# Performance work log

Measured on AMD Instinct MI355X. Metric: run time of the kernel, lower is better.

The kernel has to match this reference:

```python
import jax, jax.numpy as jnp
import numpy as np

DIM = 768
GP_NUM = 49


def setup_inputs() -> dict:
    key = jax.random.key(0)
    ks = jax.random.split(key, 7)
    b, n, d = 8, 2048, DIM
    s = d ** -0.5
    x = jax.random.normal(ks[0], (b, n, d), dtype=jnp.float32)
    W_qkv = jax.random.normal(ks[1], (d, 3 * d), dtype=jnp.float32) * s
    b_qkv = jnp.zeros((3 * d,), dtype=jnp.float32)
    W_proj = jax.random.normal(ks[2], (d, d), dtype=jnp.float32) * s
    b_proj = jnp.zeros((d,), dtype=jnp.float32)
    W_gp = jax.random.normal(ks[3], (d, GP_NUM), dtype=jnp.float32) * s
    alpha = jax.random.normal(ks[4], (), dtype=jnp.float32)
    return {"x": x, "W_qkv": W_qkv, "b_qkv": b_qkv, "W_proj": W_proj,
            "b_proj": b_proj, "W_gp": W_gp, "alpha": alpha}


def reference(x, W_qkv, b_qkv, W_proj, b_proj, W_gp, alpha):
    d = x.shape[-1]
    scale = d ** -0.5
    qkv = x @ W_qkv + b_qkv            # [b, n, 3d]
    q, k, v = jnp.split(qkv, 3, axis=-1)
    # full n x n attention scores
    attn_scores = jnp.einsum('bnd,bmd->bnm', q, k) * scale
    # group affinity: softmax(gelu(v @ W_gp)) then outer product over groups
    gw = jax.nn.softmax(jax.nn.gelu(v @ W_gp, approximate=False), axis=-1)  # [b, n, g]
    group_weight = jnp.einsum('bng,bmg->bnm', gw, gw)  # [b, n, n]
    attn_scores = jax.nn.softmax(attn_scores * group_weight, axis=-1)
    a = jax.nn.sigmoid(alpha)
    attn_weights = (1.0 - a) * attn_scores + a * group_weight
    out = jnp.einsum('bnm,bmd->bnd', attn_weights, v)
    return out @ W_proj + b_proj
```

## Files before the change

### kernel.cpp

```cpp
#include <hip/hip_runtime.h>
#include <hip/hip_bf16.h>
#include <math.h>

#define CB 8
#define CN 2048
#define CD 768
#define CDQKV 2304
#define NG 49

typedef unsigned short ushort_t;
typedef __attribute__((ext_vector_type(8))) short bf16x8;
typedef __attribute__((ext_vector_type(4))) float f32x4;

__device__ __forceinline__ float bf2f(ushort_t u) {
    unsigned int x = ((unsigned int)u) << 16;
    return __builtin_bit_cast(float, x);
}
__device__ __forceinline__ ushort_t f2bf(float f) {
    unsigned int u = __builtin_bit_cast(unsigned int, f);
    u += 0x7fff + ((u >> 16) & 1);
    return (ushort_t)(u >> 16);
}
__device__ __forceinline__ ushort_t f2h(float f) {
    _Float16 h = (_Float16)f;
    return __builtin_bit_cast(ushort_t, h);
}
__device__ __forceinline__ float h2f(ushort_t u) {
    return (float)__builtin_bit_cast(_Float16, u);
}
__device__ __forceinline__ float sigmoidf_(float x) { return 1.f / (1.f + __expf(-x)); }

__device__ __forceinline__ void gload_lds16(const ushort_t* g, ushort_t* l) {
    __builtin_amdgcn_global_load_lds((const __attribute__((address_space(1))) void*)g,
                                     (__attribute__((address_space(3))) void*)l, 16, 0, 0);
}

__global__ void ws_fail_marker(float* out) {
    if (threadIdx.x == 0 && blockIdx.x == 0) out[0] = 31337.0f;
}

__global__ __launch_bounds__(256) void cast_bf16(const float* __restrict__ X,
                                                 ushort_t* __restrict__ XB, int n)
{
    int i = (blockIdx.x * 256 + threadIdx.x) * 8;
    if (i >= n) return;
    float4 a = *(const float4*)(X + i);
    float4 b = *(const float4*)(X + i + 4);
    ushort_t t[8];
    t[0] = f2bf(a.x); t[1] = f2bf(a.y); t[2] = f2bf(a.z); t[3] = f2bf(a.w);
    t[4] = f2bf(b.x); t[5] = f2bf(b.y); t[6] = f2bf(b.z); t[7] = f2bf(b.w);
    *(uint4*)(XB + i) = *(uint4*)t;
}

__global__ __launch_bounds__(256) void wt_kernel(const float* __restrict__ W,
                                                 ushort_t* __restrict__ WT,
                                                 int rows, int cols)
{
    __shared__ ushort_t tile[64][72];
    const int bx = blockIdx.x, by = blockIdx.y;
    const int t = threadIdx.x;
    const int r = t >> 2, cp = (t & 3) * 16;
    const float* src = W + (size_t)(by * 64 + r) * cols + bx * 64 + cp;
    ushort_t tmp[16];
#pragma unroll
    for (int i = 0; i < 16; i += 4) {
        float4 v = *(const float4*)(src + i);
        tmp[i + 0] = f2bf(v.x); tmp[i + 1] = f2bf(v.y);
        tmp[i + 2] = f2bf(v.z); tmp[i + 3] = f2bf(v.w);
    }
    *(uint4*)&tile[r][cp] = *(uint4*)tmp;
    *(uint4*)&tile[r][cp + 8] = *(uint4*)(tmp + 8);
    __syncthreads();
#pragma unroll
    for (int i = 0; i < 16; i++) tmp[i] = tile[cp + i][r];
    ushort_t* dst = WT + (size_t)(bx * 64 + r) * rows + by * 64 + cp;
    *(uint4*)dst = *(uint4*)tmp;
    *(uint4*)(dst + 8) = *(uint4*)(tmp + 8);
}

__global__ __launch_bounds__(256) void wgpt_kernel(const float* __restrict__ Wg,
                                                   ushort_t* __restrict__ WGPT)
{
    int idx = blockIdx.x * 256 + threadIdx.x;
    if (idx >= 64 * CD) return;
    int gg = idx / CD, k = idx % CD;
    WGPT[idx] = (gg < NG) ? f2bf(Wg[(size_t)k * NG + gg]) : (ushort_t)0;
}

#define GEN_STAGE(dstA_, dstB_, kt_, Abase_, Bbase_, lda_, ldb_) do {          \
    _Pragma("unroll")                                                          \
    for (int _p = 0; _p < 4; _p++) {                                           \
        int _idx = _p * 256 + tid;                                             \
        int _row = _idx >> 3;                                                  \
        int _lsl = (_idx & 7) ^ (_row & 7);                                    \
        gload_lds16((Abase_) + (size_t)_row * (lda_) + (size_t)(kt_) * 64 + _lsl * 8, \
                    (dstA_) + _idx * 8);                                       \
        gload_lds16((Bbase_) + (size_t)_row * (ldb_) + (size_t)(kt_) * 64 + _lsl * 8, \
                    (dstB_) + _idx * 8);                                       \
    } } while (0)

#define G_COMPUTE(srcA_, srcB_) do {                                           \
    _Pragma("unroll")                                                          \
    for (int _ks = 0; _ks < 2; _ks++) {                                        \
        bf16x8 _af[4], _bf[4];                                                 \
        _Pragma("unroll")                                                      \
        for (int _f = 0; _f < 4; _f++) {                                       \
            int _ra = wr * 64 + _f * 16 + c;                                   \
            int _pa = (_ks * 4 + g) ^ (_ra & 7);                               \
            _af[_f] = *(const bf16x8*)((srcA_) + _ra * 64 + _pa * 8);          \
            int _rb = wc * 64 + _f * 16 + c;                                   \
            int _pb = (_ks * 4 + g) ^ (_rb & 7);                               \
            _bf[_f] = *(const bf16x8*)((srcB_) + _rb * 64 + _pb * 8);          \
        }                                                                      \
        _Pragma("unroll")                                                      \
        for (int _mf = 0; _mf < 4; _mf++)                                      \
            _Pragma("unroll")                                                  \
            for (int _nf = 0; _nf < 4; _nf++)                                  \
                acc[_mf * 4 + _nf] = __builtin_amdgcn_mfma_f32_16x16x32_bf16(  \
                    _af[_mf], _bf[_nf], acc[_mf * 4 + _nf], 0, 0, 0);          \
    } } while (0)

#define STAGE_A128(dst_, base_, ld_, kt_) do {                                 \
    _Pragma("unroll")                                                          \
    for (int _p = 0; _p < 4; _p++) {                                           \
        int _idx = _p * 256 + tid;                                             \
        int _row = _idx >> 3;                                                  \
        int _lsl = (_idx & 7) ^ (_row & 7);                                    \
        gload_lds16((base_) + (size_t)_row * (ld_) + (size_t)(kt_) * 64 + _lsl * 8, \
                    (dst_) + _idx * 8);                                        \
    } } while (0)

#define STAGE_B64(dst_, base_, ld_, kt_) do {                                  \
    _Pragma("unroll")                                                          \
    for (int _p = 0; _p < 2; _p++) {                                           \
        int _idx = _p * 256 + tid;                                             \
        int _row = _idx >> 3;                                                  \
        int _lsl = (_idx & 7) ^ (_row & 7);                                    \
        gload_lds16((base_) + (size_t)_row * (ld_) + (size_t)(kt_) * 64 + _lsl * 8, \
                    (dst_) + _idx * 8);                                        \
    } } while (0)

#define N64_COMPUTE(srcA_, srcB_) do {                                         \
    _Pragma("unroll")                                                          \
    for (int _ks = 0; _ks < 2; _ks++) {                                        \
        bf16x8 _af[2], _bf[4];                                                 \
        _Pragma("unroll")                                                      \
        for (int _f = 0; _f < 2; _f++) {                                       \
            int _ra = w * 32 + _f * 16 + c;                                    \
            int _pa = (_ks * 4 + g) ^ (_ra & 7);                               \
            _af[_f] = *(const bf16x8*)((srcA_) + _ra * 64 + _pa * 8);          \
        }                                                                      \
        _Pragma("unroll")                                                      \
        for (int _f = 0; _f < 4; _f++) {                                       \
            int _rb = _f * 16 + c;                                             \
            int _pb = (_ks * 4 + g) ^ (_rb & 7);                               \
            _bf[_f] = *(const bf16x8*)((srcB_) + _rb * 64 + _pb * 8);          \
        }                                                                      \
        _Pragma("unroll")                                                      \
        for (int _mf = 0; _mf < 2; _mf++)                                      \
            _Pragma("unroll")                                                  \
            for (int _nf = 0; _nf < 4; _nf++)                                  \
                acc[_mf * 4 + _nf] = __builtin_amdgcn_mfma_f32_16x16x32_bf16(  \
                    _af[_mf], _bf[_nf], acc[_mf * 4 + _nf], 0, 0, 0);          \
    } } while (0)

template <int OUTMODE>
__global__ __launch_bounds__(256, 2) void mfma_gemm(
    const ushort_t* __restrict__ Ag, const ushort_t* __restrict__ Bg,
    const float* __restrict__ bias,
    ushort_t* __restrict__ Qd, ushort_t* __restrict__ Kd, ushort_t* __restrict__ Vd,
    float* __restrict__ OUT)
{
    __shared__ __align__(16) ushort_t As[2][128 * 64];
    __shared__ __align__(16) ushort_t Bs[2][128 * 64];
    const int tid = threadIdx.x;
    const int lane = tid & 63;
    const int w = tid >> 6;
    const int c = lane & 15, g = lane >> 4;
    const int wr = w >> 1, wc = w & 1;
    const int m0 = blockIdx.x * 128;
    const int n0 = blockIdx.y * 128;
    const ushort_t* Ab = Ag + (size_t)m0 * CD;
    const ushort_t* Bb = Bg + (size_t)n0 * CD;

    f32x4 acc[16];
#pragma unroll
    for (int i = 0; i < 16; i++) acc[i] = (f32x4){0.f, 0.f, 0.f, 0.f};

    GEN_STAGE(As[0], Bs[0], 0, Ab, Bb, CD, CD);
    __syncthreads();
#pragma unroll 1
    for (int kt = 0; kt < 12; kt++) {
        const int cur = kt & 1;
        if (kt < 11) GEN_STAGE(As[cur ^ 1], Bs[cur ^ 1], kt + 1, Ab, Bb, CD, CD);
        G_COMPUTE(As[cur], Bs[cur]);
        __syncthreads();
    }

    if (OUTMODE == 0) {
        const int seg = n0 / CD;
        const int nl0 = n0 % CD;
        ushort_t* dst = (seg == 0) ? Qd : (seg == 1) ? Kd : Vd;
#pragma unroll
        for (int nf = 0; nf < 4; nf++) {
            float bv = bias[n0 + wc * 64 + nf * 16 + c];
            int n = nl0 + wc * 64 + nf * 16 + c;
#pragma unroll
            for (int mf = 0; mf < 4; mf++) {
#pragma unroll
                for (int r = 0; r < 4; r++) {
                    int m = m0 + wr * 64 + mf * 16 + g * 4 + r;
                    dst[(size_t)m * CD + n] = f2bf(acc[mf * 4 + nf][r] + bv);
                }
            }
        }
    } else {
#pragma unroll
        for (int nf = 0; nf < 4; nf++) {
            int n = n0 + wc * 64 + nf * 16 + c;
            float bv = bias[n];
#pragma unroll
            for (int mf = 0; mf < 4; mf++) {
#pragma unroll
                for (int r = 0; r < 4; r++) {
                    int m = m0 + wr * 64 + mf * 16 + g * 4 + r;
                    OUT[(size_t)m * CD + n] = acc[mf * 4 + nf][r] + bv;
                }
            }
        }
    }
}

__global__ __launch_bounds__(256, 2) void gw_gemm(
    const ushort_t* __restrict__ Vb, const ushort_t* __restrict__ WGPT,
    ushort_t* __restrict__ GWP, ushort_t* __restrict__ GWT)
{
    __shared__ __align__(16) ushort_t As[2][128 * 64];
    __shared__ __align__(16) ushort_t Bs[2][64 * 64];
    const int tid = threadIdx.x;
    const int lane = tid & 63;
    const int w = tid >> 6;
    const int c = lane & 15, g = lane >> 4;
    const int row0 = blockIdx.x * 128;
    const ushort_t* Ab = Vb + (size_t)row0 * CD;

    f32x4 acc[8];
#pragma unroll
    for (int i = 0; i < 8; i++) acc[i] = (f32x4){0.f, 0.f, 0.f, 0.f};

    STAGE_A128(As[0], Ab, CD, 0);
    STAGE_B64(Bs[0], WGPT, CD, 0);
    __syncthreads();
#pragma unroll 1
    for (int kt = 0; kt < 12; kt++) {
        const int cur = kt & 1;
        if (kt < 11) {
            STAGE_A128(As[cur ^ 1], Ab, CD, kt + 1);
            STAGE_B64(Bs[cur ^ 1], WGPT, CD, kt + 1);
        }
        N64_COMPUTE(As[cur], Bs[cur]);
        __syncthreads();
    }

    float gl[2][4][4];
#pragma unroll
    for (int mf = 0; mf < 2; mf++)
#pragma unroll
        for (int nf = 0; nf < 4; nf++) {
            int col = nf * 16 + c;
#pragma unroll
            for (int rr = 0; rr < 4; rr++) {
                float xx = acc[mf * 4 + nf][rr];
                float ge = 0.5f * xx * (1.f + erff(xx * 0.7071067811865475f));
                gl[mf][nf][rr] = (col < NG) ? ge : -1e30f;
            }
        }
#pragma unroll
    for (int mf = 0; mf < 2; mf++) {
#pragma unroll
        for (int rr = 0; rr < 4; rr++) {
            float m = fmaxf(fmaxf(gl[mf][0][rr], gl[mf][1][rr]),
                            fmaxf(gl[mf][2][rr], gl[mf][3][rr]));
#pragma unroll
            for (int s = 1; s < 16; s <<= 1) m = fmaxf(m, __shfl_xor(m, s, 64));
            float ssum = 0.f;
#pragma unroll
            for (int nf = 0; nf < 4; nf++) {
                int col = nf * 16 + c;
                float e = (col < NG) ? __expf(gl[mf][nf][rr] - m) : 0.f;
                gl[mf][nf][rr] = e;
                ssum += e;
            }
#pragma unroll
            for (int s = 1; s < 16; s <<= 1) ssum += __shfl_xor(ssum, s, 64);
            float inv = 1.f / ssum;
            int row = row0 + w * 32 + mf * 16 + g * 4 + rr;
            int bb = row >> 11, nn = row & 2047;
#pragma unroll
            for (int nf = 0; nf < 4; nf++) {
                int col = nf * 16 + c;
                ushort_t wv = f2bf(gl[mf][nf][rr] * inv);
                GWP[(size_t)row * 64 + col] = wv;
                GWT[((size_t)bb * 64 + col) * CN + nn] = wv;
            }
        }
    }
}

__global__ __launch_bounds__(256, 2) void z_gemm(
    const ushort_t* __restrict__ VT, const ushort_t* __restrict__ GWT,
    ushort_t* __restrict__ ZT)
{
    __shared__ __align__(16) ushort_t As[2][128 * 64];
    __shared__ __align__(16) ushort_t Bs[2][64 * 64];
    const int tid = threadIdx.x;
    const int lane = tid & 63;
    const int w = tid >> 6;
    const int c = lane & 15, g = lane >> 4;
    const int b = blockIdx.y;
    const int m0 = blockIdx.x * 128;
    const ushort_t* Ab = VT + ((size_t)b * CD + m0) * CN;
    const ushort_t* Bb = GWT + (size_t)b * 64 * CN;

    f32x4 acc[8];
#pragma unroll
    for (int i = 0; i < 8; i++) acc[i] = (f32x4){0.f, 0.f, 0.f, 0.f};

    STAGE_A128(As[0], Ab, CN, 0);
    STAGE_B64(Bs[0], Bb, CN, 0);
    __syncthreads();
#pragma unroll 1
    for (int kt = 0; kt < 32; kt++) {
        const int cur = kt & 1;
        if (kt < 31) {
            STAGE_A128(As[cur ^ 1], Ab, CN, kt + 1);
            STAGE_B64(Bs[cur ^ 1], Bb, CN, kt + 1);
        }
        N64_COMPUTE(As[cur], Bs[cur]);
        __syncthreads();
    }

#pragma unroll
    for (int mf = 0; mf < 2; mf++)
#pragma unroll
        for (int nf = 0; nf < 4; nf++) {
            int col = nf * 16 + c;
#pragma unroll
            for (int rr = 0; rr < 4; rr++) {
                int row = m0 + w * 32 + mf * 16 + g * 4 + rr;
                ZT[((size_t)b * CD + row) * 64 + col] = f2bf(acc[mf * 4 + nf][rr]);
            }
        }
}

__global__ __launch_bounds__(256, 2) void s_gemm(
    const ushort_t* __restrict__ Qb, const ushort_t* __restrict__ Kb,
    const ushort_t* __restrict__ GWP, ushort_t* __restrict__ S)
{
    __shared__ __align__(16) ushort_t As[2][128 * 64];
    __shared__ __align__(16) ushort_t Bs[2][128 * 64];
    const int tid = threadIdx.x;
    const int lane = tid & 63;
    const int w = tid >> 6;
    const int c = lane & 15, g = lane >> 4;
    const int wr = w >> 1, wc = w & 1;
    const int b = blockIdx.z;
    const int m0 = blockIdx.x * 128;
    const int n0 = blockIdx.y * 128;
    const ushort_t* Ab = Qb + ((size_t)b * CN + m0) * CD;
    const ushort_t* Bb = Kb + ((size_t)b * CN + n0) * CD;

    f32x4 acc[16], gacc[16];
#pragma unroll
    for (int i = 0; i < 16; i++) {
        acc[i] = (f32x4){0.f, 0.f, 0.f, 0.f};
        gacc[i] = (f32x4){0.f, 0.f, 0.f, 0.f};
    }

    GEN_STAGE(As[0], Bs[0], 0, Ab, Bb, CD, CD);

    {
        const ushort_t* Gq = GWP + ((size_t)b * CN + m0) * 64;
        const ushort_t* Gk = GWP + ((size_t)b * CN + n0) * 64;
        bf16x8 gqf[2][4], gkf[2][4];
#pragma unroll
        for (int ks = 0; ks < 2; ks++)
#pragma unroll
            for (int f = 0; f < 4; f++) {
                gqf[ks][f] = *(const bf16x8*)(Gq + (size_t)(wr * 64 + f * 16 + c) * 64 + ks * 32 + g * 8);
                gkf[ks][f] = *(const bf16x8*)(Gk + (size_t)(wc * 64 + f * 16 + c) * 64 + ks * 32 + g * 8);
            }
#pragma unroll
        for (int ks = 0; ks < 2; ks++)
#pragma unroll
            for (int mf = 0; mf < 4; mf++)
#pragma unroll
                for (int nf = 0; nf < 4; nf++)
                    gacc[mf * 4 + nf] = __builtin_amdgcn_mfma_f32_16x16x32_bf16(
                        gqf[ks][mf], gkf[ks][nf], gacc[mf * 4 + nf], 0, 0, 0);
    }

    __syncthreads();
#pragma unroll 1
    for (int kt = 0; kt < 12; kt++) {
        const int cur = kt & 1;
        if (kt < 11) GEN_STAGE(As[cur ^ 1], Bs[cur ^ 1], kt + 1, Ab, Bb, CD, CD);
        G_COMPUTE(As[cur], Bs[cur]);
        __syncthreads();
    }

    ushort_t* Sb = S + ((size_t)b * CN + m0) * CN + n0;
    const float scale = 0.03608439182435161f;
#pragma unroll
    for (int nf = 0; nf < 4; nf++) {
        int n = wc * 64 + nf * 16 + c;
#pragma unroll
        for (int mf = 0; mf < 4; mf++) {
#pragma unroll
            for (int r = 0; r < 4; r++) {
                int m = wr * 64 + mf * 16 + g * 4 + r;
                float z = acc[mf * 4 + nf][r] * scale * gacc[mf * 4 + nf][r];
                Sb[(size_t)m * CN + n] = f2h(z);
            }
        }
    }
}

__global__ __launch_bounds__(256) void softmax_rows(ushort_t* __restrict__ SP)
{
    const int lane = threadIdx.x & 63;
    const int row = blockIdx.x * 4 + (threadIdx.x >> 6);
    ushort_t* rp = SP + (size_t)row * CN;

    float v[32];
    float mx = -1e30f;
#pragma unroll
    for (int ch = 0; ch < 4; ch++) {
        uint4 u = *(const uint4*)(rp + ch * 512 + lane * 8);
        const unsigned int uu[4] = {u.x, u.y, u.z, u.w};
#pragma unroll
        for (int j = 0; j < 4; j++) {
            float a = h2f((ushort_t)(uu[j] & 0xffff));
            float bq = h2f((ushort_t)(uu[j] >> 16));
            v[ch * 8 + j * 2] = a;
            v[ch * 8 + j * 2 + 1] = bq;
            mx = fmaxf(mx, fmaxf(a, bq));
        }
    }
#pragma unroll
    for (int s = 32; s > 0; s >>= 1) mx = fmaxf(mx, __shfl_xor(mx, s, 64));
    float sum = 0.f;
#pragma unroll
    for (int i = 0; i < 32; i++) {
        v[i] = __expf(v[i] - mx);
        sum += v[i];
    }
#pragma unroll
    for (int s = 32; s > 0; s >>= 1) sum += __shfl_xor(sum, s, 64);
    float inv = 1.f / sum;
#pragma unroll
    for (int ch = 0; ch < 4; ch++) {
        ushort_t t[8];
#pragma unroll
        for (int j = 0; j < 8; j++) t[j] = f2bf(v[ch * 8 + j] * inv);
        *(uint4*)(rp + ch * 512 + lane * 8) = *(uint4*)t;
    }
}

__global__ __launch_bounds__(256, 2) void pv_gemm(
    const ushort_t* __restrict__ P, const ushort_t* __restrict__ VT,
    const ushort_t* __restrict__ GWP, const ushort_t* __restrict__ ZT,
    const float* __restrict__ alpha_p, ushort_t* __restrict__ OP)
{
    __shared__ __align__(16) ushort_t As[2][128 * 64];
    __shared__ __align__(16) ushort_t Bs[2][128 * 64];
    const int tid = threadIdx.x;
    const int lane = tid & 63;
    const int w = tid >> 6;
    const int c = lane & 15, g = lane >> 4;
    const int wr = w >> 1, wc = w & 1;
    const int b = blockIdx.z;
    const int m0 = blockIdx.x * 128;
    const int n0 = blockIdx.y * 128;
    const ushort_t* Ab = P + ((size_t)b * CN + m0) * CN;
    const ushort_t* Bb = VT + ((size_t)b * CD + n0) * CN;

    f32x4 acc[16], zacc[16];
#pragma unroll
    for (int i = 0; i < 16; i++) {
        acc[i] = (f32x4){0.f, 0.f, 0.f, 0.f};
        zacc[i] = (f32x4){0.f, 0.f, 0.f, 0.f};
    }

    GEN_STAGE(As[0], Bs[0], 0, Ab, Bb, CN, CN);

    {
        const ushort_t* Gq = GWP + ((size_t)b * CN + m0) * 64;
        const ushort_t* Zt = ZT + (size_t)b * CD * 64;
        bf16x8 zaf[2][4], zbf[2][4];
#pragma unroll
        for (int ks = 0; ks < 2; ks++)
#pragma unroll
            for (int f = 0; f < 4; f++) {
                zaf[ks][f] = *(const bf16x8*)(Gq + (size_t)(wr * 64 + f * 16 + c) * 64 + ks * 32 + g * 8);
                zbf[ks][f] = *(const bf16x8*)(Zt + (size_t)(n0 + wc * 64 + f * 16 + c) * 64 + ks * 32 + g * 8);
            }
#pragma unroll
        for (int ks = 0; ks < 2; ks++)
#pragma unroll
            for (int mf = 0; mf < 4; mf++)
#pragma unroll
                for (int nf = 0; nf < 4; nf++)
                    zacc[mf * 4 + nf] = __builtin_amdgcn_mfma_f32_16x16x32_bf16(
                        zaf[ks][mf], zbf[ks][nf], zacc[mf * 4 + nf], 0, 0, 0);
    }

    __syncthreads();
#pragma unroll 1
    for (int kt = 0; kt < 32; kt++) {
        const int cur = kt & 1;
        if (kt < 31) GEN_STAGE(As[cur ^ 1], Bs[cur ^ 1], kt + 1, Ab, Bb, CN, CN);
        G_COMPUTE(As[cur], Bs[cur]);
        __syncthreads();
    }

    const float aa = sigmoidf_(alpha_p[0]);
    ushort_t* OPb = OP + ((size_t)b * CN + m0) * CD;
#pragma unroll
    for (int nf = 0; nf < 4; nf++) {
        int n = n0 + wc * 64 + nf * 16 + c;
#pragma unroll
        for (int mf = 0; mf < 4; mf++) {
#pragma unroll
            for (int r = 0; r < 4; r++) {
                int m = wr * 64 + mf * 16 + g * 4 + r;
                OPb[(size_t)m * CD + n] =
                    f2bf((1.f - aa) * acc[mf * 4 + nf][r] + aa * zacc[mf * 4 + nf][r]);
            }
        }
    }
}

__global__ __launch_bounds__(256) void vt_transpose(const ushort_t* __restrict__ VB,
                                                    ushort_t* __restrict__ VT)
{
    __shared__ ushort_t tile[64][72];
    const int bx = blockIdx.x, by = blockIdx.y, b = blockIdx.z;
    const int t = threadIdx.x;
    const int r = t >> 2, cp = (t & 3) * 16;
    const ushort_t* src = VB + ((size_t)b * CN + bx * 64 + r) * CD + by * 64 + cp;
    *(uint4*)&tile[r][cp] = *(const uint4*)src;
    *(uint4*)&tile[r][cp + 8] = *(const uint4*)(src + 8);
    __syncthreads();
    ushort_t tmp[16];
#pragma unroll
    for (int i = 0; i < 16; i++) tmp[i] = tile[cp + i][r];
    ushort_t* dst = VT + ((size_t)b * CD + by * 64 + r) * CN + bx * 64 + cp;
    *(uint4*)dst = *(uint4*)tmp;
    *(uint4*)(dst + 8) = *(uint4*)(tmp + 8);
}

extern "C" void kernel_launch(void* const* d_in, const int* in_sizes, int n_in,
                              void* d_out, int out_size, void* d_ws, size_t ws_size,
                              hipStream_t stream) {
    const float* x      = (const float*)d_in[0];
    const float* W_qkv  = (const float*)d_in[1];
    const float* b_qkv  = (const float*)d_in[2];
    const float* W_proj = (const float*)d_in[3];
    const float* b_proj = (const float*)d_in[4];
    const float* W_gp   = (const float*)d_in[5];
    const float* alpha  = (const float*)d_in[6];
    float* out = (float*)d_out;

    const size_t BND    = (size_t)CB * CN * CD;
    const size_t SZ_BF  = BND * 2;
    const size_t SZ_WPT = (size_t)CD * CD * 2;
    const size_t SZ_GWP = (size_t)CB * CN * 64 * 2;
    const size_t SZ_GWT = (size_t)CB * 64 * CN * 2;
    const size_t SZ_ZT  = (size_t)CB * CD * 64 * 2;
    const size_t SZ_WGPT= (size_t)64 * CD * 2;
    const size_t SZ_SP  = (size_t)CB * CN * CN * 2;
    const size_t need = 5 * SZ_BF + SZ_WPT + SZ_GWP + SZ_GWT + SZ_ZT + SZ_WGPT + SZ_SP;
    if (ws_size < need) {
        ws_fail_marker<<<1, 1, 0, stream>>>(out);
        return;
    }
    char* p = (char*)d_ws;
    ushort_t* qb   = (ushort_t*)p; p += SZ_BF;
    ushort_t* kb   = (ushort_t*)p; p += SZ_BF;
    ushort_t* vb   = (ushort_t*)p; p += SZ_BF;
    ushort_t* vt   = (ushort_t*)p; p += SZ_BF;
    ushort_t* opb  = (ushort_t*)p; p += SZ_BF;
    ushort_t* wpt  = (ushort_t*)p; p += SZ_WPT;
    ushort_t* gwp  = (ushort_t*)p; p += SZ_GWP;
    ushort_t* gwt  = (ushort_t*)p; p += SZ_GWT;
    ushort_t* zt   = (ushort_t*)p; p += SZ_ZT;
    ushort_t* wgpt = (ushort_t*)p; p += SZ_WGPT;
    ushort_t* sp   = (ushort_t*)p; p += SZ_SP;
    ushort_t* xb  = sp;
    ushort_t* wqt = sp + BND;

    cast_bf16<<<dim3((int)(BND / 8 / 256)), 256, 0, stream>>>(x, xb, (int)BND);
    wt_kernel<<<dim3(36, 12), 256, 0, stream>>>(W_qkv, wqt, CD, CDQKV);
    wt_kernel<<<dim3(12, 12), 256, 0, stream>>>(W_proj, wpt, CD, CD);
    wgpt_kernel<<<dim3(192), 256, 0, stream>>>(W_gp, wgpt);
    mfma_gemm<0><<<dim3(128, 18), 256, 0, stream>>>(xb, wqt, b_qkv, qb, kb, vb, nullptr);
    gw_gemm<<<dim3(128), 256, 0, stream>>>(vb, wgpt, gwp, gwt);
    vt_transpose<<<dim3(32, 12, 8), 256, 0, stream>>>(vb, vt);
    z_gemm<<<dim3(6, 8), 256, 0, stream>>>(vt, gwt, zt);
    s_gemm<<<dim3(16, 16, 8), 256, 0, stream>>>(qb, kb, gwp, sp);
    softmax_rows<<<dim3(4096), 256, 0, stream>>>(sp);
    pv_gemm<<<dim3(16, 6, 8), 256, 0, stream>>>(sp, vt, gwp, zt, alpha, opb);
    mfma_gemm<1><<<dim3(128, 6), 256, 0, stream>>>(opb, wpt, b_proj, nullptr, nullptr, nullptr, out);
}
```

Baseline: 364.2 us.

## Fold group term into PV GEMM via padded K and use 256x256 GEMM tiles

Adds a 256x256-tile, 512-thread bf16 MFMA GEMM with a two-stage prefetch, explicit waitcnt barriers, priority hints and XCD-aware block remapping. It replaces the QKV, PV and output projection GEMMs. The softmax now scales by (1-a) and writes a*gw into 64 extra columns of a padded score buffer (row stride 2112). z_gemm writes into matching padded columns of V^T, so the group-weight contribution becomes part of a single K=2112 GEMM instead of a separate fused pass. The larger tiles should raise reuse, at the cost of fewer blocks (192 for PV and projection) and heavier register and LDS pressure.

Result: no change. 361.0 us (-0.9%).

```diff
diff --git a/kernel.cpp b/kernel.cpp
--- a/kernel.cpp
+++ b/kernel.cpp
@@ -7,6 +7,7 @@
 #define CD 768
 #define CDQKV 2304
 #define NG 49
+#define SLD 2112
 
 typedef unsigned short ushort_t;
 typedef __attribute__((ext_vector_type(8))) short bf16x8;
@@ -85,6 +86,143 @@
     if (idx >= 64 * CD) return;
     int gg = idx / CD, k = idx % CD;
     WGPT[idx] = (gg < NG) ? f2bf(Wg[(size_t)k * NG + gg]) : (ushort_t)0;
+}
+
+#define STAGE256(dstA_, dstB_, kt_) do {                                       \
+    _Pragma("unroll")                                                          \
+    for (int _p = 0; _p < 4; _p++) {                                           \
+        int _idx = _p * 512 + tid;                                             \
+        int _row = _idx >> 3;                                                  \
+        int _lsl = (_idx & 7) ^ (_row & 7);                                    \
+        gload_lds16(Ab + (size_t)_row * LDA + (size_t)(kt_) * 64 + _lsl * 8,   \
+                    (dstA_) + _idx * 8);                                       \
+    }                                                                          \
+    _Pragma("unroll")                                                          \
+    for (int _p = 0; _p < 4; _p++) {                                           \
+        int _idx = _p * 512 + tid;                                             \
+        int _row = _idx >> 3;                                                  \
+        int _lsl = (_idx & 7) ^ (_row & 7);                                    \
+        gload_lds16(Bb + (size_t)_row * LDB + (size_t)(kt_) * 64 + _lsl * 8,   \
+                    (dstB_) + _idx * 8);                                       \
+    } } while (0)
+
+template <int OUTMODE, int NK, int LDA, int LDB>
+__global__ __launch_bounds__(512, 2) void gemm256(
+    const ushort_t* __restrict__ Ag, const ushort_t* __restrict__ Bg,
+    const float* __restrict__ bias,
+    ushort_t* __restrict__ Qd, ushort_t* __restrict__ Kd, ushort_t* __restrict__ Vd,
+    ushort_t* __restrict__ OB, float* __restrict__ OF)
+{
+    __shared__ __align__(16) ushort_t bufA[2][256 * 64];
+    __shared__ __align__(16) ushort_t bufB[2][256 * 64];
+
+    const int tid = threadIdx.x;
+    const int lane = tid & 63;
+    const int w = tid >> 6;
+    const int c = lane & 15, g = lane >> 4;
+    const int wr = w >> 2, wc = w & 3;
+
+    const int per = gridDim.x >> 3;
+    const int idx = (blockIdx.x & 7) * per + (blockIdx.x >> 3);
+    const int mb = idx & 63;
+    const int nb = idx >> 6;
+    const int m0 = mb * 256;
+    const int n0 = nb * 256;
+
+    const ushort_t* Ab = Ag + (size_t)m0 * LDA;
+    const ushort_t* Bb = (OUTMODE == 2)
+        ? Bg + ((size_t)(m0 >> 11) * CD + n0) * LDB
+        : Bg + (size_t)n0 * LDB;
+
+    f32x4 acc[8][4];
+#pragma unroll
+    for (int i = 0; i < 8; i++)
+#pragma unroll
+        for (int j = 0; j < 4; j++) acc[i][j] = (f32x4){0.f, 0.f, 0.f, 0.f};
+
+    STAGE256(bufA[0], bufB[0], 0);
+    STAGE256(bufA[1], bufB[1], 1);
+
+#pragma unroll 1
+    for (int kt = 0; kt < NK; kt++) {
+        const int cur = kt & 1;
+        asm volatile("s_waitcnt vmcnt(8)" ::: "memory");
+        __builtin_amdgcn_s_barrier();
+
+        bf16x8 af[2][8], bf[2][4];
+#pragma unroll
+        for (int ks = 0; ks < 2; ks++) {
+#pragma unroll
+            for (int mf = 0; mf < 8; mf++) {
+                int ra = wr * 128 + mf * 16 + c;
+                int pa = (ks * 4 + g) ^ (ra & 7);
+                af[ks][mf] = *(const bf16x8*)(&bufA[cur][0] + ra * 64 + pa * 8);
+            }
+#pragma unroll
+            for (int nf = 0; nf < 4; nf++) {
+                int rb = wc * 64 + nf * 16 + c;
+                int pb = (ks * 4 + g) ^ (rb & 7);
+                bf[ks][nf] = *(const bf16x8*)(&bufB[cur][0] + rb * 64 + pb * 8);
+            }
+        }
+        asm volatile("s_waitcnt lgkmcnt(0)" ::: "memory");
+        __builtin_amdgcn_s_barrier();
+        if (kt + 2 < NK) STAGE256(bufA[cur], bufB[cur], kt + 2);
+
+        __builtin_amdgcn_s_setprio(1);
+#pragma unroll
+        for (int ks = 0; ks < 2; ks++)
+#pragma unroll
+            for (int mf = 0; mf < 8; mf++)
+#pragma unroll
+                for (int nf = 0; nf < 4; nf++)
+                    acc[mf][nf] = __builtin_amdgcn_mfma_f32_16x16x32_bf16(
+                        af[ks][mf], bf[ks][nf], acc[mf][nf], 0, 0, 0);
+        __builtin_amdgcn_s_setprio(0);
+    }
+
+    if (OUTMODE == 0) {
+        const int seg = n0 / CD;
+        const int nl0 = n0 % CD;
+        ushort_t* dst = (seg == 0) ? Qd : (seg == 1) ? Kd : Vd;
+#pragma unroll
+        for (int nf = 0; nf < 4; nf++) {
+            float bv = bias[n0 + wc * 64 + nf * 16 + c];
+            int n = nl0 + wc * 64 + nf * 16 + c;
+#pragma unroll
+            for (int mf = 0; mf < 8; mf++)
+#pragma unroll
+                for (int r = 0; r < 4; r++) {
+                    int m = m0 + wr * 128 + mf * 16 + g * 4 + r;
+                    dst[(size_t)m * CD + n] = f2bf(acc[mf][nf][r] + bv);
+                }
+        }
+    } else if (OUTMODE == 1) {
+#pragma unroll
+        for (int nf = 0; nf < 4; nf++) {
+            int n = n0 + wc * 64 + nf * 16 + c;
+            float bv = bias[n];
+#pragma unroll
+            for (int mf = 0; mf < 8; mf++)
+#pragma unroll
+                for (int r = 0; r < 4; r++) {
+                    int m = m0 + wr * 128 + mf * 16 + g * 4 + r;
+                    OF[(size_t)m * CD + n] = acc[mf][nf][r] + bv;
+                }
+        }
+    } else {
+#pragma unroll
+        for (int nf = 0; nf < 4; nf++) {
+            int n = n0 + wc * 64 + nf * 16 + c;
+#pragma unroll
+            for (int mf = 0; mf < 8; mf++)
+#pragma unroll
+                for (int r = 0; r < 4; r++) {
+                    int m = m0 + wr * 128 + mf * 16 + g * 4 + r;
+                    OB[(size_t)m * CD + n] = f2bf(acc[mf][nf][r]);
+                }
+        }
+    }
 }
 
 #define GEN_STAGE(dstA_, dstB_, kt_, Abase_, Bbase_, lda_, ldb_) do {          \
@@ -164,73 +302,6 @@
                     _af[_mf], _bf[_nf], acc[_mf * 4 + _nf], 0, 0, 0);          \
     } } while (0)
 
-template <int OUTMODE>
-__global__ __launch_bounds__(256, 2) void mfma_gemm(
-    const ushort_t* __restrict__ Ag, const ushort_t* __restrict__ Bg,
-    const float* __restrict__ bias,
-    ushort_t* __restrict__ Qd, ushort_t* __restrict__ Kd, ushort_t* __restrict__ Vd,
-    float* __restrict__ OUT)
-{
-    __shared__ __align__(16) ushort_t As[2][128 * 64];
-    __shared__ __align__(16) ushort_t Bs[2][128 * 64];
-    const int tid = threadIdx.x;
-    const int lane = tid & 63;
-    const int w = tid >> 6;
-    const int c = lane & 15, g = lane >> 4;
-    const int wr = w >> 1, wc = w & 1;
-    const int m0 = blockIdx.x * 128;
-    const int n0 = blockIdx.y * 128;
-    const ushort_t* Ab = Ag + (size_t)m0 * CD;
-    const ushort_t* Bb = Bg + (size_t)n0 * CD;
-
-    f32x4 acc[16];
-#pragma unroll
-    for (int i = 0; i < 16; i++) acc[i] = (f32x4){0.f, 0.f, 0.f, 0.f};
-
-    GEN_STAGE(As[0], Bs[0], 0, Ab, Bb, CD, CD);
-    __syncthreads();
-#pragma unroll 1
-    for (int kt = 0; kt < 12; kt++) {
-        const int cur = kt & 1;
-        if (kt < 11) GEN_STAGE(As[cur ^ 1], Bs[cur ^ 1], kt + 1, Ab, Bb, CD, CD);
-        G_COMPUTE(As[cur], Bs[cur]);
-        __syncthreads();
-    }
-
-    if (OUTMODE == 0) {
-        const int seg = n0 / CD;
-        const int nl0 = n0 % CD;
-        ushort_t* dst = (seg == 0) ? Qd : (seg == 1) ? Kd : Vd;
-#pragma unroll
-        for (int nf = 0; nf < 4; nf++) {
-            float bv = bias[n0 + wc * 64 + nf * 16 + c];
-            int n = nl0 + wc * 64 + nf * 16 + c;
-#pragma unroll
-            for (int mf = 0; mf < 4; mf++) {
-#pragma unroll
-                for (int r = 0; r < 4; r++) {
-                    int m = m0 + wr * 64 + mf * 16 + g * 4 + r;
-                    dst[(size_t)m * CD + n] = f2bf(acc[mf * 4 + nf][r] + bv);
-                }
-            }
-        }
-    } else {
-#pragma unroll
-        for (int nf = 0; nf < 4; nf++) {
-            int n = n0 + wc * 64 + nf * 16 + c;
-            float bv = bias[n];
-#pragma unroll
-            for (int mf = 0; mf < 4; mf++) {
-#pragma unroll
-                for (int r = 0; r < 4; r++) {
-                    int m = m0 + wr * 64 + mf * 16 + g * 4 + r;
-                    OUT[(size_t)m * CD + n] = acc[mf * 4 + nf][r] + bv;
-                }
-            }
-        }
-    }
-}
-
 __global__ __launch_bounds__(256, 2) void gw_gemm(
     const ushort_t* __restrict__ Vb, const ushort_t* __restrict__ WGPT,
     ushort_t* __restrict__ GWP, ushort_t* __restrict__ GWT)
@@ -308,8 +379,7 @@
 }
 
 __global__ __launch_bounds__(256, 2) void z_gemm(
-    const ushort_t* __restrict__ VT, const ushort_t* __restrict__ GWT,
-    ushort_t* __restrict__ ZT)
+    ushort_t* __restrict__ VTt, const ushort_t* __restrict__ GWT)
 {
     __shared__ __align__(16) ushort_t As[2][128 * 64];
     __shared__ __align__(16) ushort_t Bs[2][64 * 64];
@@ -319,21 +389,21 @@
     const int c = lane & 15, g = lane >> 4;
     const int b = blockIdx.y;
     const int m0 = blockIdx.x * 128;
-    const ushort_t* Ab = VT + ((size_t)b * CD + m0) * CN;
+    const ushort_t* Ab = VTt + ((size_t)b * CD + m0) * SLD;
     const ushort_t* Bb = GWT + (size_t)b * 64 * CN;
 
     f32x4 acc[8];
 #pragma unroll
     for (int i = 0; i < 8; i++) acc[i] = (f32x4){0.f, 0.f, 0.f, 0.f};
 
-    STAGE_A128(As[0], Ab, CN, 0);
+    STAGE_A128(As[0], Ab, SLD, 0);
     STAGE_B64(Bs[0], Bb, CN, 0);
     __syncthreads();
 #pragma unroll 1
     for (int kt = 0; kt < 32; kt++) {
         const int cur = kt & 1;
         if (kt < 31) {
-            STAGE_A128(As[cur ^ 1], Ab, CN, kt + 1);
+            STAGE_A128(As[cur ^ 1], Ab, SLD, kt + 1);
             STAGE_B64(Bs[cur ^ 1], Bb, CN, kt + 1);
         }
         N64_COMPUTE(As[cur], Bs[cur]);
@@ -348,7 +418,7 @@
 #pragma unroll
             for (int rr = 0; rr < 4; rr++) {
                 int row = m0 + w * 32 + mf * 16 + g * 4 + rr;
-                ZT[((size_t)b * CD + row) * 64 + col] = f2bf(acc[mf * 4 + nf][rr]);
+                VTt[((size_t)b * CD + row) * SLD + 2048 + col] = f2bf(acc[mf * 4 + nf][rr]);
             }
         }
 }
@@ -409,7 +479,7 @@
         __syncthreads();
     }
 
-    ushort_t* Sb = S + ((size_t)b * CN + m0) * CN + n0;
+    ushort_t* Sb = S + ((size_t)b * CN + m0) * SLD + n0;
     const float scale = 0.03608439182435161f;
 #pragma unroll
     for (int nf = 0; nf < 4; nf++) {
@@ -420,17 +490,19 @@
             for (int r = 0; r < 4; r++) {
                 int m = wr * 64 + mf * 16 + g * 4 + r;
                 float z = acc[mf * 4 + nf][r] * scale * gacc[mf * 4 + nf][r];
-                Sb[(size_t)m * CN + n] = f2h(z);
-            }
-        }
-    }
-}
-
-__global__ __launch_bounds__(256) void softmax_rows(ushort_t* __restrict__ SP)
+                Sb[(size_t)m * SLD + n] = f2h(z);
+            }
+        }
+    }
+}
+
+__global__ __launch_bounds__(256) void softmax_rows(ushort_t* __restrict__ SP,
+                                                    const ushort_t* __restrict__ GWP,
+                                                    const float* __restrict__ alpha_p)
 {
     const int lane = threadIdx.x & 63;
     const int row = blockIdx.x * 4 + (threadIdx.x >> 6);
-    ushort_t* rp = SP + (size_t)row * CN;
+    ushort_t* rp = SP + (size_t)row * SLD;
 
     float v[32];
     float mx = -1e30f;
@@ -457,92 +529,26 @@
     }
 #pragma unroll
     for (int s = 32; s > 0; s >>= 1) sum += __shfl_xor(sum, s, 64);
-    float inv = 1.f / sum;
+    const float aa = sigmoidf_(alpha_p[0]);
+    float sc = (1.f - aa) / sum;
 #pragma unroll
     for (int ch = 0; ch < 4; ch++) {
         ushort_t t[8];
 #pragma unroll
-        for (int j = 0; j < 8; j++) t[j] = f2bf(v[ch * 8 + j] * inv);
+        for (int j = 0; j < 8; j++) t[j] = f2bf(v[ch * 8 + j] * sc);
         *(uint4*)(rp + ch * 512 + lane * 8) = *(uint4*)t;
     }
-}
-
-__global__ __launch_bounds__(256, 2) void pv_gemm(
-    const ushort_t* __restrict__ P, const ushort_t* __restrict__ VT,
-    const ushort_t* __restrict__ GWP, const ushort_t* __restrict__ ZT,
-    const float* __restrict__ alpha_p, ushort_t* __restrict__ OP)
-{
-    __shared__ __align__(16) ushort_t As[2][128 * 64];
-    __shared__ __align__(16) ushort_t Bs[2][128 * 64];
-    const int tid = threadIdx.x;
-    const int lane = tid & 63;
-    const int w = tid >> 6;
-    const int c = lane & 15, g = lane >> 4;
-    const int wr = w >> 1, wc = w & 1;
-    const int b = blockIdx.z;
-    const int m0 = blockIdx.x * 128;
-    const int n0 = blockIdx.y * 128;
-    const ushort_t* Ab = P + ((size_t)b * CN + m0) * CN;
-    const ushort_t* Bb = VT + ((size_t)b * CD + n0) * CN;
-
-    f32x4 acc[16], zacc[16];
-#pragma unroll
-    for (int i = 0; i < 16; i++) {
-        acc[i] = (f32x4){0.f, 0.f, 0.f, 0.f};
-        zacc[i] = (f32x4){0.f, 0.f, 0.f, 0.f};
-    }
-
-    GEN_STAGE(As[0], Bs[0], 0, Ab, Bb, CN, CN);
-
-    {
-        const ushort_t* Gq = GWP + ((size_t)b * CN + m0) * 64;
-        const ushort_t* Zt = ZT + (size_t)b * CD * 64;
-        bf16x8 zaf[2][4], zbf[2][4];
-#pragma unroll
-        for (int ks = 0; ks < 2; ks++)
-#pragma unroll
-            for (int f = 0; f < 4; f++) {
-                zaf[ks][f] = *(const bf16x8*)(Gq + (size_t)(wr * 64 + f * 16 + c) * 64 + ks * 32 + g * 8);
-                zbf[ks][f] = *(const bf16x8*)(Zt + (size_t)(n0 + wc * 64 + f * 16 + c) * 64 + ks * 32 + g * 8);
-            }
-#pragma unroll
-        for (int ks = 0; ks < 2; ks++)
-#pragma unroll
-            for (int mf = 0; mf < 4; mf++)
-#pragma unroll
-                for (int nf = 0; nf < 4; nf++)
-                    zacc[mf * 4 + nf] = __builtin_amdgcn_mfma_f32_16x16x32_bf16(
-                        zaf[ks][mf], zbf[ks][nf], zacc[mf * 4 + nf], 0, 0, 0);
-    }
-
-    __syncthreads();
-#pragma unroll 1
-    for (int kt = 0; kt < 32; kt++) {
-        const int cur = kt & 1;
-        if (kt < 31) GEN_STAGE(As[cur ^ 1], Bs[cur ^ 1], kt + 1, Ab, Bb, CN, CN);
-        G_COMPUTE(As[cur], Bs[cur]);
-        __syncthreads();
-    }
-
-    const float aa = sigmoidf_(alpha_p[0]);
-    ushort_t* OPb = OP + ((size_t)b * CN + m0) * CD;
-#pragma unroll
-    for (int nf = 0; nf < 4; nf++) {
-        int n = n0 + wc * 64 + nf * 16 + c;
-#pragma unroll
-        for (int mf = 0; mf < 4; mf++) {
-#pragma unroll
-            for (int r = 0; r < 4; r++) {
-                int m = wr * 64 + mf * 16 + g * 4 + r;
-                OPb[(size_t)m * CD + n] =
-                    f2bf((1.f - aa) * acc[mf * 4 + nf][r] + aa * zacc[mf * 4 + nf][r]);
-            }
-        }
+    if (lane < 8) {
+        const ushort_t* gp = GWP + (size_t)row * 64 + lane * 8;
+        ushort_t t[8];
+#pragma unroll
+        for (int j = 0; j < 8; j++) t[j] = f2bf(aa * bf2f(gp[j]));
+        *(uint4*)(rp + 2048 + lane * 8) = *(uint4*)t;
     }
 }
 
 __global__ __launch_bounds__(256) void vt_transpose(const ushort_t* __restrict__ VB,
-                                                    ushort_t* __restrict__ VT)
+                                                    ushort_t* __restrict__ VTt)
 {
     __shared__ ushort_t tile[64][72];
     const int bx = blockIdx.x, by = blockIdx.y, b = blockIdx.z;
@@ -555,7 +561,7 @@
     ushort_t tmp[16];
 #pragma unroll
     for (int i = 0; i < 16; i++) tmp[i] = tile[cp + i][r];
-    ushort_t* dst = VT + ((size_t)b * CD + by * 64 + r) * CN + bx * 64 + cp;
+    ushort_t* dst = VTt + ((size_t)b * CD + by * 64 + r) * SLD + bx * 64 + cp;
     *(uint4*)dst = *(uint4*)tmp;
     *(uint4*)(dst + 8) = *(uint4*)(tmp + 8);
 }
@@ -574,13 +580,13 @@
 
     const size_t BND    = (size_t)CB * CN * CD;
     const size_t SZ_BF  = BND * 2;
+    const size_t SZ_VT  = (size_t)CB * CD * SLD * 2;
     const size_t SZ_WPT = (size_t)CD * CD * 2;
     const size_t SZ_GWP = (size_t)CB * CN * 64 * 2;
     const size_t SZ_GWT = (size_t)CB * 64 * CN * 2;
-    const size_t SZ_ZT  = (size_t)CB * CD * 64 * 2;
     const size_t SZ_WGPT= (size_t)64 * CD * 2;
-    const size_t SZ_SP  = (size_t)CB * CN * CN * 2;
-    const size_t need = 5 * SZ_BF + SZ_WPT + SZ_GWP + SZ_GWT + SZ_ZT + SZ_WGPT + SZ_SP;
+    const size_t SZ_SP  = (size_t)CB * CN * SLD * 2;
+    const size_t need = 4 * SZ_BF + SZ_VT + SZ_WPT + SZ_GWP + SZ_GWT + SZ_WGPT + SZ_SP;
     if (ws_size < need) {
         ws_fail_marker<<<1, 1, 0, stream>>>(out);
         return;
@@ -589,12 +595,11 @@
     ushort_t* qb   = (ushort_t*)p; p += SZ_BF;
     ushort_t* kb   = (ushort_t*)p; p += SZ_BF;
     ushort_t* vb   = (ushort_t*)p; p += SZ_BF;
-    ushort_t* vt   = (ushort_t*)p; p += SZ_BF;
     ushort_t* opb  = (ushort_t*)p; p += SZ_BF;
+    ushort_t* vtb  = (ushort_t*)p; p += SZ_VT;
     ushort_t* wpt  = (ushort_t*)p; p += SZ_WPT;
     ushort_t* gwp  = (ushort_t*)p; p += SZ_GWP;
     ushort_t* gwt  = (ushort_t*)p; p += SZ_GWT;
-    ushort_t* zt   = (ushort_t*)p; p += SZ_ZT;
     ushort_t* wgpt = (ushort_t*)p; p += SZ_WGPT;
     ushort_t* sp   = (ushort_t*)p; p += SZ_SP;
     ushort_t* xb  = sp;
@@ -604,12 +609,15 @@
     wt_kernel<<<dim3(36, 12), 256, 0, stream>>>(W_qkv, wqt, CD, CDQKV);
     wt_kernel<<<dim3(12, 12), 256, 0, stream>>>(W_proj, wpt, CD, CD);
     wgpt_kernel<<<dim3(192), 256, 0, stream>>>(W_gp, wgpt);
-    mfma_gemm<0><<<dim3(128, 18), 256, 0, stream>>>(xb, wqt, b_qkv, qb, kb, vb, nullptr);
+    gemm256<0, 12, CD, CD><<<dim3(576), 512, 0, stream>>>(
+        xb, wqt, b_qkv, qb, kb, vb, nullptr, nullptr);
     gw_gemm<<<dim3(128), 256, 0, stream>>>(vb, wgpt, gwp, gwt);
-    vt_transpose<<<dim3(32, 12, 8), 256, 0, stream>>>(vb, vt);
-    z_gemm<<<dim3(6, 8), 256, 0, stream>>>(vt, gwt, zt);
+    vt_transpose<<<dim3(32, 12, 8), 256, 0, stream>>>(vb, vtb);
+    z_gemm<<<dim3(6, 8), 256, 0, stream>>>(vtb, gwt);
     s_gemm<<<dim3(16, 16, 8), 256, 0, stream>>>(qb, kb, gwp, sp);
-    softmax_rows<<<dim3(4096), 256, 0, stream>>>(sp);
-    pv_gemm<<<dim3(16, 6, 8), 256, 0, stream>>>(sp, vt, gwp, zt, alpha, opb);
-    mfma_gemm<1><<<dim3(128, 6), 256, 0, stream>>>(opb, wpt, b_proj, nullptr, nullptr, nullptr, out);
-}
+    softmax_rows<<<dim3(4096), 256, 0, stream>>>(sp, gwp, alpha);
+    gemm256<2, 33, SLD, SLD><<<dim3(192), 512, 0, stream>>>(
+        sp, vtb, nullptr, nullptr, nullptr, nullptr, opb, nullptr);
+    gemm256<1, 12, CD, CD><<<dim3(192), 512, 0, stream>>>(
+        opb, wpt, b_proj, nullptr, nullptr, nullptr, nullptr, out);
+}
```
